# Optimization experiments

Hardware: AMD Instinct MI355X
Metric: run time of the kernel (lower is better)

## Reference

```python
import jax, jax.numpy as jnp
import numpy as np

B, N, F_IN, UNITS, E, MAX_VIEW = 4, 10000, 64, 64, 160000, 3
C = F_IN + UNITS  # concat channel dim (num_embedding)


def setup_inputs() -> dict:
    key = jax.random.key(0)
    ks = jax.random.split(key, 8)
    inputs = jax.random.normal(ks[0], (B, N, F_IN), jnp.float32)
    hx = jax.random.normal(ks[1], (B, N, UNITS), jnp.float32)
    sparse_idx = jax.random.randint(ks[2], (2, E), 0, N)          # row0=src, row1=dst
    conv_ker = jax.random.normal(ks[3], (E,), jnp.float32) * 0.1  # per-edge kernel weight
    W_ru = jax.random.normal(ks[4], (MAX_VIEW * C, 2 * UNITS), jnp.float32) * 0.05
    b_ru = jnp.zeros((2 * UNITS,), jnp.float32)
    W_c = jax.random.normal(ks[5], (MAX_VIEW * C, UNITS), jnp.float32) * 0.05
    b_c = jnp.zeros((UNITS,), jnp.float32)
    return dict(inputs=inputs, hx=hx, sparse_idx=sparse_idx, conv_ker=conv_ker,
                W_ru=W_ru, b_ru=b_ru, W_c=W_c, b_c=b_c)


def _graph_conv(x, src, dst, ker, W, b):
    """Multi-view sparse graph conv: [x, A x, A^2 x, ...] concat -> linear.
    x: (B, N, C); edge e aggregates ker[e] * x[:, src[e]] into node dst[e]."""
    views = [x]
    y = x
    for _ in range(MAX_VIEW - 1):
        msg = y[:, src, :] * ker[None, :, None]        # (B, E, C) gather + scale
        y = jnp.zeros_like(x).at[:, dst, :].add(msg)   # (B, N, C) scatter-add
        views.append(y)
    h = jnp.concatenate(views, axis=-1)                # (B, N, MAX_VIEW*C)
    return h @ W + b


def reference(inputs, hx, sparse_idx, conv_ker, W_ru, b_ru, W_c, b_c):
    src, dst = sparse_idx[0], sparse_idx[1]
    # GRU r,u gates from graph conv over concat(inputs, hx)
    x_ru = jnp.concatenate([inputs, hx], axis=-1)                      # (B, N, C)
    ru = jax.nn.sigmoid(_graph_conv(x_ru, src, dst, conv_ker, W_ru, b_ru))
    r, u = jnp.split(ru, 2, axis=-1)                                   # (B, N, UNITS) each
    # candidate state from graph conv over concat(inputs, r*hx)
    x_c = jnp.concatenate([inputs, r * hx], axis=-1)
    c = jnp.tanh(_graph_conv(x_c, src, dst, conv_ker, W_c, b_c))
    return u * hx + (1.0 - u) * c
```

## Files before the change

### kernel.cpp

```cpp
#include <hip/hip_runtime.h>
#include <hip/hip_bf16.h>
#include <math.h>

#define NB 10000
#define BB 4
#define EE 160000
#define MM (NB * BB)
#define SLOTS 64

typedef __attribute__((ext_vector_type(8))) short short8;
typedef __attribute__((ext_vector_type(4))) float floatx4;


__device__ inline unsigned pk(float a, float b) {
  __hip_bfloat16 ha = __float2bfloat16(a), hb = __float2bfloat16(b);
  unsigned short ua = *(unsigned short*)&ha, ub = *(unsigned short*)&hb;
  return (unsigned)ua | ((unsigned)ub << 16);
}

__device__ inline float bf2f(ushort u) {
  unsigned v = (unsigned)u << 16;
  return __uint_as_float(v);
}

__device__ inline ushort f2bf(float f) {
  __hip_bfloat16 h = __float2bfloat16(f);
  return *(unsigned short*)&h;
}

__device__ inline void fma8(float* a, uint4 v, float k) {
  a[0] += k * __uint_as_float(v.x << 16);
  a[1] += k * __uint_as_float(v.x & 0xffff0000u);
  a[2] += k * __uint_as_float(v.y << 16);
  a[3] += k * __uint_as_float(v.y & 0xffff0000u);
  a[4] += k * __uint_as_float(v.z << 16);
  a[5] += k * __uint_as_float(v.z & 0xffff0000u);
  a[6] += k * __uint_as_float(v.w << 16);
  a[7] += k * __uint_as_float(v.w & 0xffff0000u);
}


__global__ __launch_bounds__(256) void k_misc(
    const int* __restrict__ src, const int* __restrict__ dst,
    const float* __restrict__ ker, int* __restrict__ cnt,
    uint2* __restrict__ edges,
    const float* __restrict__ in, const float* __restrict__ hx,
    ushort* __restrict__ x,
    const float* __restrict__ Wru, const float* __restrict__ Wc,
    ushort* __restrict__ Bru, ushort* __restrict__ Bcin,
    ushort* __restrict__ Bc2) {
  int blk = blockIdx.x;
  if (blk < 625) {
    int e = blk * 256 + threadIdx.x;
    if (e < EE) {
      int n = dst[e];
      int slot = atomicAdd(&cnt[n], 1);
      if (slot < SLOTS)
        edges[(size_t)n * SLOTS + slot] =
            make_uint2((unsigned)src[e], __float_as_uint(ker[e]));
    }
  } else if (blk < 3125) {
    int tid = (blk - 625) * 256 + threadIdx.x;
    int m = tid >> 4;
    int c8 = (tid & 15) << 3;
    const float* sp = (c8 < 64) ? (in + (size_t)m * 64 + c8)
                                : (hx + (size_t)m * 64 + (c8 - 64));
    float4 f0 = *(const float4*)(sp);
    float4 f1 = *(const float4*)(sp + 4);
    uint4 o;
    o.x = pk(f0.x, f0.y); o.y = pk(f0.z, f0.w);
    o.z = pk(f1.x, f1.y); o.w = pk(f1.z, f1.w);
    *(uint4*)(x + (size_t)m * 128 + c8) = o;
  } else if (blk < 3149) {
    int t = (blk - 3125) * 256 + threadIdx.x;
    int kt = t >> 9;
    int nt = (t >> 6) & 7;
    int lane = t & 63;
    int quad = lane >> 4, lr = lane & 15;
    int colb = nt * 16 + lr;
    int kb = kt * 32 + quad * 8;
    short8 v;
#pragma unroll
    for (int j = 0; j < 8; ++j) v[j] = (short)f2bf(Wru[(size_t)(kb + j) * 128 + colb]);
    *(short8*)(Bru + (size_t)t * 8) = v;
  } else if (blk < 3155) {
    int t = (blk - 3149) * 256 + threadIdx.x;
    int ktc = t >> 8;
    int nt = (t >> 6) & 3;
    int lane = t & 63;
    int quad = lane >> 4, lr = lane & 15;
    int vv = ktc >> 1, h = ktc & 1;
    int colb = nt * 16 + lr;
    int kb = vv * 128 + h * 32 + quad * 8;
    short8 v;
#pragma unroll
    for (int j = 0; j < 8; ++j) v[j] = (short)f2bf(Wc[(size_t)(kb + j) * 64 + colb]);
    *(short8*)(Bcin + (size_t)t * 8) = v;
  } else {
    int t = (blk - 3155) * 256 + threadIdx.x;
    int ktc = t >> 8;
    int nt = (t >> 6) & 3;
    int lane = t & 63;
    int quad = lane >> 4, lr = lane & 15;
    int vv = ktc >> 1, h = ktc & 1;
    int colb = nt * 16 + lr;
    int kb = vv * 128 + 64 + h * 32 + quad * 8;
    short8 v;
#pragma unroll
    for (int j = 0; j < 8; ++j) v[j] = (short)f2bf(Wc[(size_t)(kb + j) * 64 + colb]);
    *(short8*)(Bc2 + (size_t)t * 8) = v;
  }
}


__global__ __launch_bounds__(256) void k_prop128(const ushort* __restrict__ x,
                                                 ushort* __restrict__ y,
                                                 const int* __restrict__ cnt,
                                                 const uint2* __restrict__ edges) {
  int blk = blockIdx.x;
  int b = (blk & 7) >> 1;
  int jb = ((blk >> 3) << 1) | (blk & 1);
  int w = threadIdx.x >> 6;
  int lane = threadIdx.x & 63;
  int n = jb * 4 + w;
  int g = lane >> 4;
  int o8 = (lane & 15) << 3;
  const ushort* xb = x + (size_t)b * NB * 128;
  const uint2* ebase = edges + (size_t)n * SLOTS;
  int deg = min(cnt[n], SLOTS);
  float acc[8];
#pragma unroll
  for (int j = 0; j < 8; ++j) acc[j] = 0.f;
  int i = g;
  for (; i + 12 < deg; i += 16) {
    uint2 e0 = ebase[i], e1 = ebase[i + 4], e2 = ebase[i + 8], e3 = ebase[i + 12];
    uint4 v0 = *(const uint4*)(xb + (size_t)e0.x * 128 + o8);
    uint4 v1 = *(const uint4*)(xb + (size_t)e1.x * 128 + o8);
    uint4 v2 = *(const uint4*)(xb + (size_t)e2.x * 128 + o8);
    uint4 v3 = *(const uint4*)(xb + (size_t)e3.x * 128 + o8);
    fma8(acc, v0, __uint_as_float(e0.y));
    fma8(acc, v1, __uint_as_float(e1.y));
    fma8(acc, v2, __uint_as_float(e2.y));
    fma8(acc, v3, __uint_as_float(e3.y));
  }
  for (; i < deg; i += 4) {
    uint2 e0 = ebase[i];
    uint4 v0 = *(const uint4*)(xb + (size_t)e0.x * 128 + o8);
    fma8(acc, v0, __uint_as_float(e0.y));
  }
#pragma unroll
  for (int j = 0; j < 8; ++j) {
    acc[j] += __shfl_xor(acc[j], 16);
    acc[j] += __shfl_xor(acc[j], 32);
  }
  if (g == 0) {
    uint4 o;
    o.x = pk(acc[0], acc[1]); o.y = pk(acc[2], acc[3]);
    o.z = pk(acc[4], acc[5]); o.w = pk(acc[6], acc[7]);
    *(uint4*)(y + (size_t)b * NB * 128 + (size_t)n * 128 + o8) = o;
  }
}

__global__ __launch_bounds__(256) void k_prop64(const ushort* __restrict__ x,
                                                ushort* __restrict__ y,
                                                const int* __restrict__ cnt,
                                                const uint2* __restrict__ edges) {
  int blk = blockIdx.x;
  int b = (blk & 7) >> 1;
  int jb = ((blk >> 3) << 1) | (blk & 1);
  int w = threadIdx.x >> 6;
  int lane = threadIdx.x & 63;
  int n = jb * 4 + w;
  int g = lane >> 3;
  int o8 = (lane & 7) << 3;
  const ushort* xb = x + (size_t)b * NB * 64;
  const uint2* ebase = edges + (size_t)n * SLOTS;
  int deg = min(cnt[n], SLOTS);
  float acc[8];
#pragma unroll
  for (int j = 0; j < 8; ++j) acc[j] = 0.f;
  int i = g;
  for (; i + 8 < deg; i += 16) {
    uint2 e0 = ebase[i], e1 = ebase[i + 8];
    uint4 v0 = *(const uint4*)(xb + (size_t)e0.x * 64 + o8);
    uint4 v1 = *(const uint4*)(xb + (size_t)e1.x * 64 + o8);
    fma8(acc, v0, __uint_as_float(e0.y));
    fma8(acc, v1, __uint_as_float(e1.y));
  }
  for (; i < deg; i += 8) {
    uint2 e0 = ebase[i];
    uint4 v0 = *(const uint4*)(xb + (size_t)e0.x * 64 + o8);
    fma8(acc, v0, __uint_as_float(e0.y));
  }
#pragma unroll
  for (int j = 0; j < 8; ++j) {
    acc[j] += __shfl_xor(acc[j], 8);
    acc[j] += __shfl_xor(acc[j], 16);
    acc[j] += __shfl_xor(acc[j], 32);
  }
  if (g == 0) {
    uint4 o;
    o.x = pk(acc[0], acc[1]); o.y = pk(acc[2], acc[3]);
    o.z = pk(acc[4], acc[5]); o.w = pk(acc[6], acc[7]);
    *(uint4*)(y + (size_t)b * NB * 64 + (size_t)n * 64 + o8) = o;
  }
}


__global__ __launch_bounds__(256) void k_gemm1(
    const ushort* __restrict__ x, const ushort* __restrict__ y1,
    const ushort* __restrict__ y2, const ushort* __restrict__ Bru,
    const ushort* __restrict__ Bcin, const float* __restrict__ bias,
    const float* __restrict__ hx, ushort* __restrict__ rh0,
    ushort* __restrict__ u, ushort* __restrict__ cp) {
  const int tid = threadIdx.x;
  const int lane = tid & 63;
  const int w = tid >> 6;
  const int m0 = blockIdx.x * 64 + w * 16;
  const int lr = lane & 15;
  const int quad = lane >> 4;
  const int koff = quad * 8;

  const ushort* vb[3] = {x, y1, y2};
  short8 a[12];
#pragma unroll
  for (int v = 0; v < 3; ++v)
#pragma unroll
    for (int h = 0; h < 4; ++h)
      a[v * 4 + h] = *(const short8*)(vb[v] + (size_t)(m0 + lr) * 128 + h * 32 + koff);

  const ushort* bru = Bru + (size_t)lane * 8;
  const ushort* bcin = Bcin + (size_t)lane * 8;

  floatx4 aru[8], ac[4];
#pragma unroll
  for (int nt = 0; nt < 8; ++nt) aru[nt] = {0.f, 0.f, 0.f, 0.f};
#pragma unroll
  for (int nt = 0; nt < 4; ++nt) ac[nt] = {0.f, 0.f, 0.f, 0.f};

  short8 bc[8];
#pragma unroll
  for (int nt = 0; nt < 8; ++nt) bc[nt] = *(const short8*)(bru + (size_t)nt * 512);

#pragma unroll
  for (int kt = 0; kt < 12; ++kt) {
    short8 bn[8];
    if (kt < 11) {
#pragma unroll
      for (int nt = 0; nt < 8; ++nt)
        bn[nt] = *(const short8*)(bru + (size_t)((kt + 1) * 8 + nt) * 512);
    }
#pragma unroll
    for (int nt = 0; nt < 8; ++nt)
      aru[nt] = __builtin_amdgcn_mfma_f32_16x16x32_bf16(a[kt], bc[nt], aru[nt], 0, 0, 0);
    const int h = kt & 3;
    if (h < 2) {
      const int ktc = (kt >> 2) * 2 + h;
#pragma unroll
      for (int nt = 0; nt < 4; ++nt) {
        short8 b2 = *(const short8*)(bcin + (size_t)(ktc * 4 + nt) * 512);
        ac[nt] = __builtin_amdgcn_mfma_f32_16x16x32_bf16(a[kt], b2, ac[nt], 0, 0, 0);
      }
    }
    if (kt < 11) {
#pragma unroll
      for (int nt = 0; nt < 8; ++nt) bc[nt] = bn[nt];
    }
  }

#pragma unroll
  for (int nt = 0; nt < 8; ++nt) {
    int col = nt * 16 + lr;
    float bv = bias[col];
#pragma unroll
    for (int i = 0; i < 4; ++i) {
      int m = m0 + quad * 4 + i;
      float s = 1.f / (1.f + expf(-(aru[nt][i] + bv)));
      if (nt < 4) {
        rh0[(size_t)m * 64 + col] = f2bf(s * hx[(size_t)m * 64 + col]);
      } else {
        u[(size_t)m * 64 + (col - 64)] = f2bf(s);
      }
    }
  }
#pragma unroll
  for (int nt = 0; nt < 4; ++nt) {
    int col = nt * 16 + lr;
#pragma unroll
    for (int i = 0; i < 4; ++i) {
      int m = m0 + quad * 4 + i;
      cp[(size_t)m * 64 + col] = f2bf(ac[nt][i]);
    }
  }
}


__global__ __launch_bounds__(256) void k_gemm2(
    const ushort* __restrict__ rh0, const ushort* __restrict__ rh1,
    const ushort* __restrict__ rh2, const ushort* __restrict__ Bc2,
    const float* __restrict__ bias, const ushort* __restrict__ cp,
    const ushort* __restrict__ uu, const float* __restrict__ hx,
    float* __restrict__ out) {
  const int tid = threadIdx.x;
  const int lane = tid & 63;
  const int w = tid >> 6;
  const int m0 = blockIdx.x * 64 + w * 16;
  const int lr = lane & 15;
  const int quad = lane >> 4;
  const int koff = quad * 8;

  const ushort* vb[3] = {rh0, rh1, rh2};
  short8 a[6];
#pragma unroll
  for (int v = 0; v < 3; ++v)
#pragma unroll
    for (int h = 0; h < 2; ++h)
      a[v * 2 + h] = *(const short8*)(vb[v] + (size_t)(m0 + lr) * 64 + h * 32 + koff);

  float cpv[16], uv[16], hxv[16];
#pragma unroll
  for (int nt = 0; nt < 4; ++nt)
#pragma unroll
    for (int i = 0; i < 4; ++i) {
      size_t idx = (size_t)(m0 + quad * 4 + i) * 64 + nt * 16 + lr;
      cpv[nt * 4 + i] = bf2f(cp[idx]);
      uv[nt * 4 + i] = bf2f(uu[idx]);
      hxv[nt * 4 + i] = hx[idx];
    }

  const ushort* bp = Bc2 + (size_t)lane * 8;
  floatx4 acc[4];
#pragma unroll
  for (int nt = 0; nt < 4; ++nt) acc[nt] = {0.f, 0.f, 0.f, 0.f};

  short8 bc[4];
#pragma unroll
  for (int nt = 0; nt < 4; ++nt) bc[nt] = *(const short8*)(bp + (size_t)nt * 512);

#pragma unroll
  for (int kt = 0; kt < 6; ++kt) {
    short8 bn[4];
    if (kt < 5) {
#pragma unroll
      for (int nt = 0; nt < 4; ++nt)
        bn[nt] = *(const short8*)(bp + (size_t)((kt + 1) * 4 + nt) * 512);
    }
#pragma unroll
    for (int nt = 0; nt < 4; ++nt)
      acc[nt] = __builtin_amdgcn_mfma_f32_16x16x32_bf16(a[kt], bc[nt], acc[nt], 0, 0, 0);
    if (kt < 5) {
#pragma unroll
      for (int nt = 0; nt < 4; ++nt) bc[nt] = bn[nt];
    }
  }

#pragma unroll
  for (int nt = 0; nt < 4; ++nt) {
    int col = nt * 16 + lr;
    float bv = bias[col];
#pragma unroll
    for (int i = 0; i < 4; ++i) {
      int m = m0 + quad * 4 + i;
      int j = nt * 4 + i;
      float c = tanhf(acc[nt][i] + cpv[j] + bv);
      out[(size_t)m * 64 + col] = uv[j] * hxv[j] + (1.f - uv[j]) * c;
    }
  }
}


extern "C" void kernel_launch(void* const* d_in, const int* in_sizes, int n_in,
                              void* d_out, int out_size, void* d_ws, size_t ws_size,
                              hipStream_t stream) {
  const float* d_inputs = (const float*)d_in[0];
  const float* d_hx     = (const float*)d_in[1];
  const int*   d_sidx   = (const int*)d_in[2];
  const float* d_ker    = (const float*)d_in[3];
  const float* d_Wru    = (const float*)d_in[4];
  const float* d_bru    = (const float*)d_in[5];
  const float* d_Wc     = (const float*)d_in[6];
  const float* d_bc     = (const float*)d_in[7];
  float* out = (float*)d_out;
  const int* src = d_sidx;
  const int* dst = d_sidx + EE;

  ushort* x     = (ushort*)d_ws;
  ushort* y1    = x + (size_t)MM * 128;
  ushort* y2    = y1 + (size_t)MM * 128;
  ushort* rh0   = y2 + (size_t)MM * 128;
  ushort* rh1   = rh0 + (size_t)MM * 64;
  ushort* rh2   = rh1 + (size_t)MM * 64;
  ushort* u     = rh2 + (size_t)MM * 64;
  ushort* cp    = u + (size_t)MM * 64;
  ushort* Bru   = cp + (size_t)MM * 64;
  ushort* Bcin  = Bru + 12 * 8 * 64 * 8;
  ushort* Bc2   = Bcin + 6 * 4 * 64 * 8;
  uint2*  edges = (uint2*)(Bc2 + 6 * 4 * 64 * 8);
  int*    cnt   = (int*)(edges + (size_t)NB * SLOTS);

  hipMemsetAsync(cnt, 0, NB * sizeof(int), stream);
  k_misc<<<3161, 256, 0, stream>>>(src, dst, d_ker, cnt, edges,
                                   d_inputs, d_hx, x, d_Wru, d_Wc,
                                   Bru, Bcin, Bc2);

  k_prop128<<<10000, 256, 0, stream>>>(x, y1, cnt, edges);
  k_prop128<<<10000, 256, 0, stream>>>(y1, y2, cnt, edges);
  k_gemm1<<<625, 256, 0, stream>>>(x, y1, y2, Bru, Bcin, d_bru, d_hx,
                                   rh0, u, cp);

  k_prop64<<<10000, 256, 0, stream>>>(rh0, rh1, cnt, edges);
  k_prop64<<<10000, 256, 0, stream>>>(rh1, rh2, cnt, edges);
  k_gemm2<<<625, 256, 0, stream>>>(rh0, rh1, rh2, Bc2, d_bc, cp, u, d_hx, out);
}
```

Measured before the change: 198.0 us.

## Split graph propagation into per-batch launches for cache-resident working set

Graph propagation kernels now launch once per batch element, 2500 blocks each, with the two hops of a batch back to back. Before, a single launch interleaved all four batches. Each launch now gathers only from one batch's feature slice (about 2.5 MB for 128 channels in bf16), which is meant to fit in L2/MALL and cut gather misses. The cost is 16 launches instead of 4, each with smaller grids and more tail effects.

Result: slower. 242.9 us (+22.6%).

```diff
diff --git a/kernel.cpp b/kernel.cpp
--- a/kernel.cpp
+++ b/kernel.cpp
@@ -113,19 +113,15 @@
 }
 
 
-__global__ __launch_bounds__(256) void k_prop128(const ushort* __restrict__ x,
-                                                 ushort* __restrict__ y,
+__global__ __launch_bounds__(256) void k_prop128(const ushort* __restrict__ xb,
+                                                 ushort* __restrict__ yb,
                                                  const int* __restrict__ cnt,
                                                  const uint2* __restrict__ edges) {
-  int blk = blockIdx.x;
-  int b = (blk & 7) >> 1;
-  int jb = ((blk >> 3) << 1) | (blk & 1);
   int w = threadIdx.x >> 6;
   int lane = threadIdx.x & 63;
-  int n = jb * 4 + w;
+  int n = blockIdx.x * 4 + w;
   int g = lane >> 4;
   int o8 = (lane & 15) << 3;
-  const ushort* xb = x + (size_t)b * NB * 128;
   const uint2* ebase = edges + (size_t)n * SLOTS;
   int deg = min(cnt[n], SLOTS);
   float acc[8];
@@ -157,23 +153,20 @@
     uint4 o;
     o.x = pk(acc[0], acc[1]); o.y = pk(acc[2], acc[3]);
     o.z = pk(acc[4], acc[5]); o.w = pk(acc[6], acc[7]);
-    *(uint4*)(y + (size_t)b * NB * 128 + (size_t)n * 128 + o8) = o;
-  }
-}
-
-__global__ __launch_bounds__(256) void k_prop64(const ushort* __restrict__ x,
-                                                ushort* __restrict__ y,
+    *(uint4*)(yb + (size_t)n * 128 + o8) = o;
+  }
+}
+
+
+__global__ __launch_bounds__(256) void k_prop64(const ushort* __restrict__ xb,
+                                                ushort* __restrict__ yb,
                                                 const int* __restrict__ cnt,
                                                 const uint2* __restrict__ edges) {
-  int blk = blockIdx.x;
-  int b = (blk & 7) >> 1;
-  int jb = ((blk >> 3) << 1) | (blk & 1);
   int w = threadIdx.x >> 6;
   int lane = threadIdx.x & 63;
-  int n = jb * 4 + w;
+  int n = blockIdx.x * 4 + w;
   int g = lane >> 3;
   int o8 = (lane & 7) << 3;
-  const ushort* xb = x + (size_t)b * NB * 64;
   const uint2* ebase = edges + (size_t)n * SLOTS;
   int deg = min(cnt[n], SLOTS);
   float acc[8];
@@ -202,7 +195,7 @@
     uint4 o;
     o.x = pk(acc[0], acc[1]); o.y = pk(acc[2], acc[3]);
     o.z = pk(acc[4], acc[5]); o.w = pk(acc[6], acc[7]);
-    *(uint4*)(y + (size_t)b * NB * 64 + (size_t)n * 64 + o8) = o;
+    *(uint4*)(yb + (size_t)n * 64 + o8) = o;
   }
 }
 
@@ -403,12 +396,18 @@
                                    d_inputs, d_hx, x, d_Wru, d_Wc,
                                    Bru, Bcin, Bc2);
 
-  k_prop128<<<10000, 256, 0, stream>>>(x, y1, cnt, edges);
-  k_prop128<<<10000, 256, 0, stream>>>(y1, y2, cnt, edges);
+  for (int b = 0; b < BB; ++b) {
+    size_t o = (size_t)b * NB * 128;
+    k_prop128<<<2500, 256, 0, stream>>>(x + o, y1 + o, cnt, edges);
+    k_prop128<<<2500, 256, 0, stream>>>(y1 + o, y2 + o, cnt, edges);
+  }
   k_gemm1<<<625, 256, 0, stream>>>(x, y1, y2, Bru, Bcin, d_bru, d_hx,
                                    rh0, u, cp);
 
-  k_prop64<<<10000, 256, 0, stream>>>(rh0, rh1, cnt, edges);
-  k_prop64<<<10000, 256, 0, stream>>>(rh1, rh2, cnt, edges);
+  for (int b = 0; b < BB; ++b) {
+    size_t o = (size_t)b * NB * 64;
+    k_prop64<<<2500, 256, 0, stream>>>(rh0 + o, rh1 + o, cnt, edges);
+    k_prop64<<<2500, 256, 0, stream>>>(rh1 + o, rh2 + o, cnt, edges);
+  }
   k_gemm2<<<625, 256, 0, stream>>>(rh0, rh1, rh2, Bc2, d_bc, cp, u, d_hx, out);
 }
```
